# Optimization experiments

Measured on AMD Instinct MI355X. Metric: run time of the kernel, lower is better.

## Reference

```python
import jax, jax.numpy as jnp
import numpy as np
from functools import partial

S = 4096      # total tokens (single-request prefill)
H = 32        # indexer heads
D = 128       # indexer head dim (power of 2 for Hadamard)
R = 64        # rope head dim
QLR = 1536    # q_lora_rank
HID = 2048    # hidden size
TOPK = 2048   # index_topk
EPS = 1e-6
NEG = -1e30


def fwht(x):
    """Fast Walsh-Hadamard transform over last dim, scaled by d**-0.5."""
    d = x.shape[-1]
    orig = x.shape
    x = x.reshape(-1, d)
    h = 1
    while h < d:
        x = x.reshape(-1, d // (2 * h), 2, h)
        a, b = x[:, :, 0, :], x[:, :, 1, :]
        x = jnp.stack([a + b, a - b], axis=2).reshape(-1, d)
        h *= 2
    return (x * (d ** -0.5)).reshape(orig)


def apply_rope_interleaved(x, cos, sin):
    # non-neox (interleaved pairs): (x0,x1) -> (x0*c - x1*s, x0*s + x1*c)
    xe, xo = x[..., 0::2], x[..., 1::2]
    return jnp.stack([xe * cos - xo * sin, xe * sin + xo * cos], axis=-1).reshape(x.shape)


def setup_inputs() -> dict:
    key = jax.random.key(0)
    ks = jax.random.split(key, 8)
    hidden_states = jax.random.normal(ks[0], (S, HID), dtype=jnp.float32)
    q_lora = jax.random.normal(ks[1], (S, QLR), dtype=jnp.float32)
    positions = jnp.arange(S, dtype=jnp.int32)
    Wq = jax.random.normal(ks[2], (QLR, H * D), dtype=jnp.float32) * 0.02
    Wk = jax.random.normal(ks[3], (HID, D), dtype=jnp.float32) * 0.02
    k_gamma = jnp.ones((D,), dtype=jnp.float32)
    k_beta = jnp.zeros((D,), dtype=jnp.float32)
    Wp = jax.random.normal(ks[4], (HID, H), dtype=jnp.float32) * 0.02
    return {"hidden_states": hidden_states, "q_lora": q_lora, "positions": positions,
            "Wq": Wq, "Wk": Wk, "k_gamma": k_gamma, "k_beta": k_beta, "Wp": Wp}


def _indexer_logits(hidden_states, q_lora, Wq, Wk, k_gamma, k_beta, Wp, positions):
    # q projection: [S, QLR] @ [QLR, H*D] -> [S, H, D]
    q = (q_lora @ Wq).reshape(S, H, D)
    # k projection + layernorm: [S, D]
    k = hidden_states @ Wk
    mu = jnp.mean(k, axis=-1, keepdims=True)
    var = jnp.mean(jnp.square(k - mu), axis=-1, keepdims=True)
    k = (k - mu) * jax.lax.rsqrt(var + EPS) * k_gamma + k_beta
    # RoPE on first R dims (interleaved / non-neox style)
    half = R // 2
    inv_freq = 1.0 / (10000.0 ** (jnp.arange(half, dtype=jnp.float32) * 2.0 / R))
    ang = positions.astype(jnp.float32)[:, None] * inv_freq          # [S, half]
    cos, sin = jnp.cos(ang), jnp.sin(ang)
    q = q.at[..., :R].set(apply_rope_interleaved(q[..., :R], cos[:, None, :], sin[:, None, :]))
    k = k.at[..., :R].set(apply_rope_interleaved(k[..., :R], cos, sin))
    # Hadamard activation rotation
    q = fwht(q)
    k = fwht(k)
    # per-head gate: weights_proj(x) * n_heads^-0.5 * q_scale(=1) * softmax_scale
    w = (hidden_states @ Wp) * (H ** -0.5) * (D ** -0.5)             # [S, H]
    # logits[t, s] = sum_h w[t, h] * relu(q[t, h] . k[s]); scan over heads
    k_t = k.T                                                         # [D, S]
    def head_step(acc, inp):
        qh, wh = inp                                                  # [S, D], [S]
        return acc + wh[:, None] * jax.nn.relu(qh @ k_t), None
    logits, _ = jax.lax.scan(head_step, jnp.zeros((S, S), jnp.float32),
                             (q.transpose(1, 0, 2), w.T))
    # causal mask (ks=0, ke=t+1 per token for single-request prefill)
    idx = jnp.arange(S)
    logits = jnp.where(idx[None, :] <= idx[:, None], logits, NEG)
    return logits


def reference(hidden_states, q_lora, positions, Wq, Wk, k_gamma, k_beta, Wp):
    logits = _indexer_logits(hidden_states, q_lora, Wq, Wk, k_gamma, k_beta, Wp, positions)
    vals, topk_idx = jax.lax.top_k(logits, TOPK)                      # [S, TOPK]
    topk_idx = jnp.where(vals > NEG * 0.5, topk_idx, -1).astype(jnp.int32)
    return logits, topk_idx
```

## Files before the change

kernel.cpp:

```cpp
#include <hip/hip_runtime.h>
#include <hip/hip_bf16.h>
#include <math.h>

#define S 4096
#define H 32
#define D 128
#define QLR 1536
#define HID 2048
#define TOPK_N 2048
#define NEGF (-1e30f)
#define KW_N 160

typedef __attribute__((ext_vector_type(8))) short bf16x8;
typedef __attribute__((ext_vector_type(4))) float f32x4;

__device__ __forceinline__ void async_copy16(const void* g, void* l) {
    __builtin_amdgcn_global_load_lds(
        (const __attribute__((address_space(1))) unsigned int*)g,
        (__attribute__((address_space(3))) unsigned int*)l,
        16, 0, 0);
}

__device__ __forceinline__ unsigned short bf16bits(float f) {
    __hip_bfloat16 h = __float2bfloat16(f);
    return *(unsigned short*)&h;
}

__global__ __launch_bounds__(256) void cast_bf16_kernel(
    const float* __restrict__ in, __hip_bfloat16* __restrict__ out, int n4)
{
    int i = blockIdx.x * blockDim.x + threadIdx.x;
    if (i < n4) {
        float4 v = ((const float4*)in)[i];
        ushort4 pack;
        pack.x = bf16bits(v.x);
        pack.y = bf16bits(v.y);
        pack.z = bf16bits(v.z);
        pack.w = bf16bits(v.w);
        *(ushort4*)(out + (size_t)i * 4) = pack;
    }
}

__global__ __launch_bounds__(256) void zero_f32(float* __restrict__ p, int n)
{
    int i = blockIdx.x * blockDim.x + threadIdx.x;
    if (i < n) p[i] = 0.0f;
}

__global__ __launch_bounds__(256) void transpose_cast_kernel(
    const float* __restrict__ in, __hip_bfloat16* __restrict__ out)
{
    __shared__ float sm[32][33];
    const int nb = blockIdx.x;
    const int kb = blockIdx.y;
    const int t = threadIdx.x;
    const int j = t & 31, i0 = t >> 5;
#pragma unroll
    for (int u = 0; u < 4; ++u) {
        int i = i0 + u * 8;
        sm[i][j] = in[(size_t)(kb * 32 + i) * 4096 + nb * 32 + j];
    }
    __syncthreads();
#pragma unroll
    for (int u = 0; u < 4; ++u) {
        int i = i0 + u * 8;
        out[(size_t)(nb * 32 + i) * 1536 + kb * 32 + j] = __float2bfloat16(sm[j][i]);
    }
}

__global__ __launch_bounds__(256) void build_wkpT(
    const float* __restrict__ Wk, const float* __restrict__ Wp,
    __hip_bfloat16* __restrict__ WkpT)
{
    int g = blockIdx.x * blockDim.x + threadIdx.x;
    if (g >= KW_N * HID) return;
    int n = g / HID, k = g % HID;
    float v = (n < 128) ? Wk[(size_t)k * 128 + n]
                        : Wp[(size_t)k * 32 + (n - 128)] * 0.015625f;
    WkpT[g] = __float2bfloat16(v);
}

__global__ __launch_bounds__(256, 2) void kw_mfma(
    const short* __restrict__ hb,
    const short* __restrict__ WkpT,
    float* __restrict__ kf32,
    float* __restrict__ wbuf)
{
    const int mt = blockIdx.x;
    const int kc = blockIdx.y;
    const int tid = threadIdx.x;
    const int wave = tid >> 6, lane = tid & 63, grp = lane >> 4, lm = lane & 15;
    __shared__ short As[64 * 128];
    __shared__ short Bs[KW_N * 128];

    const int rhi = tid >> 4;
    const int e = (tid & 15) ^ rhi;

#pragma unroll
    for (int it = 0; it < 4; ++it) {
        int r = it * 16 + rhi;
        async_copy16(hb + (size_t)(mt * 64 + r) * HID + kc * 128 + e * 8,
                     (void*)(As + it * 2048 + wave * 512));
    }
#pragma unroll
    for (int it = 0; it < 10; ++it) {
        int r = it * 16 + rhi;
        async_copy16(WkpT + (size_t)r * HID + kc * 128 + e * 8,
                     (void*)(Bs + it * 2048 + wave * 512));
    }
    __syncthreads();

    f32x4 acc[10] = {};
#pragma unroll
    for (int k4 = 0; k4 < 4; ++k4) {
        int ch = ((k4 << 2) + grp) ^ lm;
        bf16x8 a = *(const bf16x8*)(As + (wave * 16 + lm) * 128 + ch * 8);
#pragma unroll
        for (int n = 0; n < 10; ++n) {
            bf16x8 b = *(const bf16x8*)(Bs + (n * 16 + lm) * 128 + ch * 8);
            acc[n] = __builtin_amdgcn_mfma_f32_16x16x32_bf16(a, b, acc[n], 0, 0, 0);
        }
    }

#pragma unroll
    for (int n = 0; n < 10; ++n) {
#pragma unroll
        for (int r = 0; r < 4; ++r) {
            int row = mt * 64 + wave * 16 + grp * 4 + r;
            int col = n * 16 + lm;
            if (n < 8) atomicAdd(&kf32[(size_t)row * 128 + col], acc[n][r]);
            else       atomicAdd(&wbuf[(size_t)row * 32 + (col - 128)], acc[n][r]);
        }
    }
}

__global__ __launch_bounds__(256, 2) void gemm_bf16_bt(
    const __hip_bfloat16* __restrict__ A, const __hip_bfloat16* __restrict__ BT,
    __hip_bfloat16* __restrict__ C, int M, int N, int K)
{
    __shared__ short As[128 * 32];
    __shared__ short Bs[128 * 32];
    const int tid = threadIdx.x;
    const int wave = tid >> 6, lane = tid & 63, grp = lane >> 4, lm = lane & 15;
    const int row0 = blockIdx.y * 128, col0 = blockIdx.x * 128;
    const short* Ag = (const short*)A;
    const short* Bg = (const short*)BT;

    f32x4 acc[2][8] = {};

    for (int kc = 0; kc < K; kc += 32) {
        __syncthreads();
#pragma unroll
        for (int is = 0; is < 2; ++is) {
            int r = is * 64 + (tid >> 2);
            async_copy16(Ag + (size_t)(row0 + r) * K + kc + (tid & 3) * 8,
                         (void*)(As + is * 2048 + wave * 512));
            async_copy16(Bg + (size_t)(col0 + r) * K + kc + (tid & 3) * 8,
                         (void*)(Bs + is * 2048 + wave * 512));
        }
        __syncthreads();
        bf16x8 a0 = *(const bf16x8*)(As + (wave * 32 + lm) * 32 + grp * 8);
        bf16x8 a1 = *(const bf16x8*)(As + (wave * 32 + 16 + lm) * 32 + grp * 8);
#pragma unroll
        for (int c = 0; c < 8; ++c) {
            bf16x8 b = *(const bf16x8*)(Bs + (c * 16 + lm) * 32 + grp * 8);
            acc[0][c] = __builtin_amdgcn_mfma_f32_16x16x32_bf16(a0, b, acc[0][c], 0, 0, 0);
            acc[1][c] = __builtin_amdgcn_mfma_f32_16x16x32_bf16(a1, b, acc[1][c], 0, 0, 0);
        }
    }
#pragma unroll
    for (int t = 0; t < 2; ++t)
#pragma unroll
        for (int c = 0; c < 8; ++c)
#pragma unroll
            for (int r = 0; r < 4; ++r) {
                int rr = row0 + wave * 32 + t * 16 + grp * 4 + r;
                int cc = col0 + c * 16 + lm;
                C[(size_t)rr * N + cc] = __float2bfloat16(acc[t][c][r]);
            }
}

__global__ void sincos_table_kernel(const int* __restrict__ positions,
                                    float* __restrict__ cosT, float* __restrict__ sinT)
{
    int g = blockIdx.x * blockDim.x + threadIdx.x;
    if (g >= S * 32) return;
    int s = g >> 5;
    int p = g & 31;
    double inv = pow(10000.0, -((double)(2 * p)) / 64.0);
    double ang = (double)positions[s] * inv;
    cosT[g] = (float)cos(ang);
    sinT[g] = (float)sin(ang);
}

__global__ __launch_bounds__(128) void post_kernel(
    const void* in, int in_bf16, __hip_bfloat16* outb,
    const float* __restrict__ cosT, const float* __restrict__ sinT,
    const float* __restrict__ gamma, const float* __restrict__ beta,
    int heads, int do_ln)
{
    const int row = blockIdx.x;
    const int t = threadIdx.x;
    const int srow = row / heads;
    __shared__ float sm[128];
    __shared__ float red[2];

    float v;
    if (in_bf16) v = __bfloat162float(((const __hip_bfloat16*)in)[(size_t)row * 128 + t]);
    else         v = ((const float*)in)[(size_t)row * 128 + t];

    if (do_ln) {
        float sv = v;
#pragma unroll
        for (int o = 32; o > 0; o >>= 1) sv += __shfl_down(sv, o);
        if ((t & 63) == 0) red[t >> 6] = sv;
        __syncthreads();
        float mu = (red[0] + red[1]) * (1.0f / 128.0f);
        __syncthreads();
        float d = v - mu;
        float sq = d * d;
#pragma unroll
        for (int o = 32; o > 0; o >>= 1) sq += __shfl_down(sq, o);
        if ((t & 63) == 0) red[t >> 6] = sq;
        __syncthreads();
        float var = (red[0] + red[1]) * (1.0f / 128.0f);
        v = d * rsqrtf(var + 1e-6f) * gamma[t] + beta[t];
        __syncthreads();
    }
    sm[t] = v;
    __syncthreads();

    if (t < 32) {
        float c = cosT[(size_t)srow * 32 + t];
        float sn = sinT[(size_t)srow * 32 + t];
        float xe = sm[2 * t];
        float xo = sm[2 * t + 1];
        sm[2 * t]     = xe * c - xo * sn;
        sm[2 * t + 1] = xe * sn + xo * c;
    }
    __syncthreads();

    for (int hstep = 1; hstep < 128; hstep <<= 1) {
        int i = 0; float a = 0.f, b = 0.f;
        bool act = (t < 64);
        if (act) {
            i = ((t & ~(hstep - 1)) << 1) | (t & (hstep - 1));
            a = sm[i];
            b = sm[i + hstep];
        }
        __syncthreads();
        if (act) { sm[i] = a + b; sm[i + hstep] = a - b; }
        __syncthreads();
    }
    outb[(size_t)row * 128 + t] = __float2bfloat16(sm[t] * 0.08838834764831845f);
}

__global__ __launch_bounds__(256, 2) void logits_mfma(
    const short* __restrict__ qb,
    const short* __restrict__ kb,
    const float* __restrict__ w,
    float* __restrict__ out)
{
    const int bx = blockIdx.x, by = blockIdx.y;
    const int row0 = by * 128, col0 = bx * 128;
    const int tid = threadIdx.x;

    if (bx > by) {
        const float4 n4 = make_float4(NEGF, NEGF, NEGF, NEGF);
        int c = (tid & 31) * 4;
        for (int r = tid >> 5; r < 128; r += 8)
            *(float4*)&out[(size_t)(row0 + r) * S + col0 + c] = n4;
        return;
    }

    __shared__ short As[128 * 128];
    __shared__ short Bs[128 * 128];
    const int wave = tid >> 6, lane = tid & 63, grp = lane >> 4, lm = lane & 15;
    const int rhi = tid >> 4;
    const int e = (tid & 15) ^ rhi;

#pragma unroll
    for (int it = 0; it < 8; ++it) {
        int r = it * 16 + rhi;
        async_copy16(kb + (size_t)(col0 + r) * D + e * 8,
                     (void*)(Bs + it * 2048 + wave * 512));
    }

    f32x4 accP[2][8] = {};

    for (int h = 0; h < H; ++h) {
        __syncthreads();
#pragma unroll
        for (int it = 0; it < 8; ++it) {
            int r = it * 16 + rhi;
            async_copy16(qb + (size_t)(row0 + r) * (H * D) + h * D + e * 8,
                         (void*)(As + it * 2048 + wave * 512));
        }
        float wv[2][4];
#pragma unroll
        for (int t = 0; t < 2; ++t)
#pragma unroll
            for (int r = 0; r < 4; ++r)
                wv[t][r] = w[(size_t)(row0 + wave * 32 + t * 16 + grp * 4 + r) * H + h];
        __syncthreads();

        f32x4 accH[2][8] = {};
#pragma unroll
        for (int kc = 0; kc < 4; ++kc) {
            int ch = ((kc << 2) + grp) ^ lm;
            bf16x8 a0 = *(const bf16x8*)(As + (wave * 32 + lm) * 128 + ch * 8);
            bf16x8 a1 = *(const bf16x8*)(As + (wave * 32 + 16 + lm) * 128 + ch * 8);
#pragma unroll
            for (int c = 0; c < 8; ++c) {
                bf16x8 b = *(const bf16x8*)(Bs + (c * 16 + lm) * 128 + ch * 8);
                accH[0][c] = __builtin_amdgcn_mfma_f32_16x16x32_bf16(a0, b, accH[0][c], 0, 0, 0);
                accH[1][c] = __builtin_amdgcn_mfma_f32_16x16x32_bf16(a1, b, accH[1][c], 0, 0, 0);
            }
        }
#pragma unroll
        for (int t = 0; t < 2; ++t)
#pragma unroll
            for (int c = 0; c < 8; ++c)
#pragma unroll
                for (int r = 0; r < 4; ++r)
                    accP[t][c][r] += wv[t][r] * fmaxf(accH[t][c][r], 0.0f);
    }

#pragma unroll
    for (int t = 0; t < 2; ++t)
#pragma unroll
        for (int c = 0; c < 8; ++c)
#pragma unroll
            for (int r = 0; r < 4; ++r) {
                int rr = row0 + wave * 32 + t * 16 + grp * 4 + r;
                int cc = col0 + c * 16 + lm;
                out[(size_t)rr * S + cc] = (cc <= rr) ? accP[t][c][r] : NEGF;
            }
}

__device__ __forceinline__ unsigned mono32(float f)
{
    unsigned u = __float_as_uint(f);
    return (u & 0x80000000u) ? ~u : (u | 0x80000000u);
}

__global__ __launch_bounds__(256) void topk_select(
    const float* __restrict__ logits, float* __restrict__ out_idx)
{
    const int row = blockIdx.x;
    const int tid = threadIdx.x;
    const int valid = row + 1;
    float* orow = out_idx + (size_t)row * TOPK_N;

    if (valid <= TOPK_N) {
        for (int p = tid; p < TOPK_N; p += 256)
            orow[p] = (p < valid) ? (float)p : -1.0f;
        return;
    }

    __shared__ float vals[S];
    __shared__ unsigned hist[2048];
    __shared__ unsigned chunk[256];
    __shared__ unsigned long long sh_prefix;
    __shared__ int sh_rem;
    __shared__ unsigned sh_cnt;

    const float* lr = logits + (size_t)row * S;
    for (int j = tid; j < valid; j += 256) vals[j] = lr[j];
    if (tid == 0) { sh_prefix = 0ull; sh_rem = TOPK_N; sh_cnt = 0u; }
    __syncthreads();

    for (int rnd = 0; rnd < 4; ++rnd) {
        const int shift = 33 - 11 * rnd;
        for (int i = tid; i < 2048; i += 256) hist[i] = 0u;
        __syncthreads();
        const unsigned long long pref = sh_prefix;
        const int rem = sh_rem;
        const int hs = shift + 11;
        for (int j = tid; j < valid; j += 256) {
            unsigned long long key = (((unsigned long long)mono32(vals[j])) << 12)
                                   | (unsigned)(4095 - j);
            if ((key >> hs) == (pref >> hs))
                atomicAdd(&hist[(unsigned)(key >> shift) & 2047u], 1u);
        }
        __syncthreads();
        unsigned csum = 0;
#pragma unroll
        for (int d = 0; d < 8; ++d) csum += hist[tid * 8 + d];
        chunk[tid] = csum;
        __syncthreads();
        for (int off = 1; off < 256; off <<= 1) {
            unsigned v = (tid + off < 256) ? chunk[tid + off] : 0u;
            __syncthreads();
            chunk[tid] += v;
            __syncthreads();
        }
        unsigned A = (tid < 255) ? chunk[tid + 1] : 0u;
        for (int dd = 7; dd >= 0; --dd) {
            unsigned c = hist[tid * 8 + dd];
            if (c && A < (unsigned)rem && (unsigned)rem <= A + c) {
                sh_prefix = pref | ((unsigned long long)(tid * 8 + dd) << shift);
                sh_rem = rem - (int)A;
            }
            A += c;
        }
        __syncthreads();
    }

    const unsigned long long Kstar = sh_prefix;
    for (int j = tid; j < valid; j += 256) {
        unsigned long long key = (((unsigned long long)mono32(vals[j])) << 12)
                               | (unsigned)(4095 - j);
        if (key >= Kstar) {
            unsigned p = atomicAdd(&sh_cnt, 1u);
            orow[p] = (float)j;
        }
    }
}

extern "C" void kernel_launch(void* const* d_in, const int* in_sizes, int n_in,
                              void* d_out, int out_size, void* d_ws, size_t ws_size,
                              hipStream_t stream)
{
    const float* hidden    = (const float*)d_in[0];
    const float* q_lora    = (const float*)d_in[1];
    const int*   positions = (const int*)d_in[2];
    const float* Wq        = (const float*)d_in[3];
    const float* Wk        = (const float*)d_in[4];
    const float* k_gamma   = (const float*)d_in[5];
    const float* k_beta    = (const float*)d_in[6];
    const float* Wp        = (const float*)d_in[7];

    char* ws = (char*)d_ws;
    size_t off = 0;
    __hip_bfloat16* qb16 = (__hip_bfloat16*)(ws + off); off += (size_t)S * H * D * 2;
    __hip_bfloat16* qlb  = (__hip_bfloat16*)(ws + off); off += (size_t)S * QLR * 2;
    __hip_bfloat16* WqT  = (__hip_bfloat16*)(ws + off); off += (size_t)(H * D) * QLR * 2;
    __hip_bfloat16* hb   = (__hip_bfloat16*)(ws + off); off += (size_t)S * HID * 2;
    __hip_bfloat16* WkpT = (__hip_bfloat16*)(ws + off); off += (size_t)KW_N * HID * 2;
    float* kf32 = (float*)(ws + off); off += (size_t)S * D * 4;
    __hip_bfloat16* kb16 = (__hip_bfloat16*)(ws + off); off += (size_t)S * D * 2;
    float* wbuf = (float*)(ws + off); off += (size_t)S * H * 4;
    float* cosT = (float*)(ws + off); off += (size_t)S * 32 * 4;
    float* sinT = (float*)(ws + off); off += (size_t)S * 32 * 4;

    float* out_logits = (float*)d_out;
    float* out_idx = out_logits + (size_t)S * S;

    cast_bf16_kernel<<<(S * QLR / 4 + 255) / 256, 256, 0, stream>>>(q_lora, qlb, S * QLR / 4);
    transpose_cast_kernel<<<dim3((H * D) / 32, QLR / 32), 256, 0, stream>>>(Wq, WqT);

    gemm_bf16_bt<<<dim3((H * D) / 128, S / 128), 256, 0, stream>>>(
        qlb, WqT, qb16, S, H * D, QLR);

    cast_bf16_kernel<<<(S * HID / 4 + 255) / 256, 256, 0, stream>>>(hidden, hb, S * HID / 4);
    build_wkpT<<<(KW_N * HID + 255) / 256, 256, 0, stream>>>(Wk, Wp, WkpT);
    zero_f32<<<(S * D + 255) / 256, 256, 0, stream>>>(kf32, S * D);
    zero_f32<<<(S * H + 255) / 256, 256, 0, stream>>>(wbuf, S * H);
    kw_mfma<<<dim3(S / 64, HID / 128), 256, 0, stream>>>(
        (const short*)hb, (const short*)WkpT, kf32, wbuf);

    sincos_table_kernel<<<(S * 32) / 256, 256, 0, stream>>>(positions, cosT, sinT);

    post_kernel<<<S, 128, 0, stream>>>(kf32, 0, kb16, cosT, sinT, k_gamma, k_beta, 1, 1);
    post_kernel<<<S * H, 128, 0, stream>>>(qb16, 1, qb16, cosT, sinT, nullptr, nullptr, H, 0);

    logits_mfma<<<dim3(S / 128, S / 128), 256, 0, stream>>>(
        (const short*)qb16, (const short*)kb16, wbuf, out_logits);

    topk_select<<<S, 256, 0, stream>>>(out_logits, out_idx);
}
```

Measured before the change: 507.1 us.

## Rewrite post-processing as wave-per-row shuffles; retile logits kernel with register-resident K

The LayerNorm/RoPE/Hadamard post kernel now runs one row per wavefront, each lane holding two elements. The reductions and butterfly stages use xor shuffles instead of shared memory and many block barriers. The logits kernel switches to 64x128 tiles with a 2x2 wave layout and loads the K fragments into registers once, so the inner head loop skips re-reading B from LDS. Occupancy hint rises to 3 blocks per CU. The cost is more register pressure and a finer causal-skip granularity, which adds blocks.

```diff
diff --git a/kernel.cpp b/kernel.cpp
--- a/kernel.cpp
+++ b/kernel.cpp
@@ -24,6 +24,11 @@
 __device__ __forceinline__ unsigned short bf16bits(float f) {
     __hip_bfloat16 h = __float2bfloat16(f);
     return *(unsigned short*)&h;
+}
+
+__device__ __forceinline__ float bits2f(unsigned short u) {
+    unsigned v = ((unsigned)u) << 16;
+    return __uint_as_float(v);
 }
 
 __global__ __launch_bounds__(256) void cast_bf16_kernel(
@@ -193,89 +198,91 @@
     sinT[g] = (float)sin(ang);
 }
 
-__global__ __launch_bounds__(128) void post_kernel(
-    const void* in, int in_bf16, __hip_bfloat16* outb,
+__global__ __launch_bounds__(256) void post_wave(
+    const void* __restrict__ in, int in_bf16, __hip_bfloat16* __restrict__ outb,
     const float* __restrict__ cosT, const float* __restrict__ sinT,
     const float* __restrict__ gamma, const float* __restrict__ beta,
-    int heads, int do_ln)
-{
-    const int row = blockIdx.x;
-    const int t = threadIdx.x;
+    int heads, int do_ln, int nrows)
+{
+    const int row = blockIdx.x * 4 + (threadIdx.x >> 6);
+    if (row >= nrows) return;
+    const int l = threadIdx.x & 63;
     const int srow = row / heads;
-    __shared__ float sm[128];
-    __shared__ float red[2];
-
-    float v;
-    if (in_bf16) v = __bfloat162float(((const __hip_bfloat16*)in)[(size_t)row * 128 + t]);
-    else         v = ((const float*)in)[(size_t)row * 128 + t];
+
+    float a, b;
+    if (in_bf16) {
+        unsigned pr = ((const unsigned*)in)[(size_t)row * 64 + l];
+        a = bits2f((unsigned short)(pr & 0xffff));
+        b = bits2f((unsigned short)(pr >> 16));
+    } else {
+        float2 v = ((const float2*)in)[(size_t)row * 64 + l];
+        a = v.x; b = v.y;
+    }
 
     if (do_ln) {
-        float sv = v;
-#pragma unroll
-        for (int o = 32; o > 0; o >>= 1) sv += __shfl_down(sv, o);
-        if ((t & 63) == 0) red[t >> 6] = sv;
-        __syncthreads();
-        float mu = (red[0] + red[1]) * (1.0f / 128.0f);
-        __syncthreads();
-        float d = v - mu;
-        float sq = d * d;
-#pragma unroll
-        for (int o = 32; o > 0; o >>= 1) sq += __shfl_down(sq, o);
-        if ((t & 63) == 0) red[t >> 6] = sq;
-        __syncthreads();
-        float var = (red[0] + red[1]) * (1.0f / 128.0f);
-        v = d * rsqrtf(var + 1e-6f) * gamma[t] + beta[t];
-        __syncthreads();
-    }
-    sm[t] = v;
-    __syncthreads();
-
-    if (t < 32) {
-        float c = cosT[(size_t)srow * 32 + t];
-        float sn = sinT[(size_t)srow * 32 + t];
-        float xe = sm[2 * t];
-        float xo = sm[2 * t + 1];
-        sm[2 * t]     = xe * c - xo * sn;
-        sm[2 * t + 1] = xe * sn + xo * c;
-    }
-    __syncthreads();
-
-    for (int hstep = 1; hstep < 128; hstep <<= 1) {
-        int i = 0; float a = 0.f, b = 0.f;
-        bool act = (t < 64);
-        if (act) {
-            i = ((t & ~(hstep - 1)) << 1) | (t & (hstep - 1));
-            a = sm[i];
-            b = sm[i + hstep];
-        }
-        __syncthreads();
-        if (act) { sm[i] = a + b; sm[i + hstep] = a - b; }
-        __syncthreads();
-    }
-    outb[(size_t)row * 128 + t] = __float2bfloat16(sm[t] * 0.08838834764831845f);
-}
-
-__global__ __launch_bounds__(256, 2) void logits_mfma(
+        float s = a + b;
+#pragma unroll
+        for (int o = 1; o < 64; o <<= 1) s += __shfl_xor(s, o);
+        float mu = s * (1.0f / 128.0f);
+        float da = a - mu, db = b - mu;
+        float sq = da * da + db * db;
+#pragma unroll
+        for (int o = 1; o < 64; o <<= 1) sq += __shfl_xor(sq, o);
+        float rs = rsqrtf(sq * (1.0f / 128.0f) + 1e-6f);
+        float2 g = ((const float2*)gamma)[l];
+        float2 bt = ((const float2*)beta)[l];
+        a = da * rs * g.x + bt.x;
+        b = db * rs * g.y + bt.y;
+    }
+
+    if (l < 32) {
+        float c = cosT[(size_t)srow * 32 + l];
+        float sn = sinT[(size_t)srow * 32 + l];
+        float xe = a, xo = b;
+        a = xe * c - xo * sn;
+        b = xe * sn + xo * c;
+    }
+
+    {
+        float na = a + b, nb = a - b;
+        a = na; b = nb;
+    }
+#pragma unroll
+    for (int m = 1; m < 64; m <<= 1) {
+        float pa = __shfl_xor(a, m);
+        float pb = __shfl_xor(b, m);
+        if (l & m) { a = pa - a; b = pb - b; }
+        else       { a = a + pa; b = b + pb; }
+    }
+
+    const float sc = 0.08838834764831845f;
+    unsigned outp = (unsigned)bf16bits(a * sc) | ((unsigned)bf16bits(b * sc) << 16);
+    ((unsigned*)outb)[(size_t)row * 64 + l] = outp;
+}
+
+__global__ __launch_bounds__(256, 3) void logits_mfma(
     const short* __restrict__ qb,
     const short* __restrict__ kb,
     const float* __restrict__ w,
     float* __restrict__ out)
 {
-    const int bx = blockIdx.x, by = blockIdx.y;
-    const int row0 = by * 128, col0 = bx * 128;
+    const int bx = blockIdx.x;
+    const int by = blockIdx.y;
+    const int row0 = by * 64, col0 = bx * 128;
     const int tid = threadIdx.x;
 
-    if (bx > by) {
+    if (2 * bx > by) {
         const float4 n4 = make_float4(NEGF, NEGF, NEGF, NEGF);
         int c = (tid & 31) * 4;
-        for (int r = tid >> 5; r < 128; r += 8)
+        for (int r = tid >> 5; r < 64; r += 8)
             *(float4*)&out[(size_t)(row0 + r) * S + col0 + c] = n4;
         return;
     }
 
-    __shared__ short As[128 * 128];
+    __shared__ short As[64 * 128];
     __shared__ short Bs[128 * 128];
     const int wave = tid >> 6, lane = tid & 63, grp = lane >> 4, lm = lane & 15;
+    const int wr = wave >> 1, wc = wave & 1;
     const int rhi = tid >> 4;
     const int e = (tid & 15) ^ rhi;
 
@@ -285,13 +292,22 @@
         async_copy16(kb + (size_t)(col0 + r) * D + e * 8,
                      (void*)(Bs + it * 2048 + wave * 512));
     }
-
-    f32x4 accP[2][8] = {};
+    __syncthreads();
+
+    bf16x8 bfrag[4][4];
+#pragma unroll
+    for (int c = 0; c < 4; ++c)
+#pragma unroll
+        for (int kc = 0; kc < 4; ++kc)
+            bfrag[c][kc] = *(const bf16x8*)(
+                Bs + (wc * 64 + c * 16 + lm) * 128 + (((kc << 2) + grp) ^ lm) * 8);
+
+    f32x4 accP[2][4] = {};
 
     for (int h = 0; h < H; ++h) {
         __syncthreads();
 #pragma unroll
-        for (int it = 0; it < 8; ++it) {
+        for (int it = 0; it < 4; ++it) {
             int r = it * 16 + rhi;
             async_copy16(qb + (size_t)(row0 + r) * (H * D) + h * D + e * 8,
                          (void*)(As + it * 2048 + wave * 512));
@@ -301,26 +317,25 @@
         for (int t = 0; t < 2; ++t)
 #pragma unroll
             for (int r = 0; r < 4; ++r)
-                wv[t][r] = w[(size_t)(row0 + wave * 32 + t * 16 + grp * 4 + r) * H + h];
-        __syncthreads();
-
-        f32x4 accH[2][8] = {};
+                wv[t][r] = w[(size_t)(row0 + wr * 32 + t * 16 + grp * 4 + r) * H + h];
+        __syncthreads();
+
+        f32x4 accH[2][4] = {};
 #pragma unroll
         for (int kc = 0; kc < 4; ++kc) {
             int ch = ((kc << 2) + grp) ^ lm;
-            bf16x8 a0 = *(const bf16x8*)(As + (wave * 32 + lm) * 128 + ch * 8);
-            bf16x8 a1 = *(const bf16x8*)(As + (wave * 32 + 16 + lm) * 128 + ch * 8);
-#pragma unroll
-            for (int c = 0; c < 8; ++c) {
-                bf16x8 b = *(const bf16x8*)(Bs + (c * 16 + lm) * 128 + ch * 8);
-                accH[0][c] = __builtin_amdgcn_mfma_f32_16x16x32_bf16(a0, b, accH[0][c], 0, 0, 0);
-                accH[1][c] = __builtin_amdgcn_mfma_f32_16x16x32_bf16(a1, b, accH[1][c], 0, 0, 0);
+            bf16x8 a0 = *(const bf16x8*)(As + (wr * 32 + lm) * 128 + ch * 8);
+            bf16x8 a1 = *(const bf16x8*)(As + (wr * 32 + 16 + lm) * 128 + ch * 8);
+#pragma unroll
+            for (int c = 0; c < 4; ++c) {
+                accH[0][c] = __builtin_amdgcn_mfma_f32_16x16x32_bf16(a0, bfrag[c][kc], accH[0][c], 0, 0, 0);
+                accH[1][c] = __builtin_amdgcn_mfma_f32_16x16x32_bf16(a1, bfrag[c][kc], accH[1][c], 0, 0, 0);
             }
         }
 #pragma unroll
         for (int t = 0; t < 2; ++t)
 #pragma unroll
-            for (int c = 0; c < 8; ++c)
+            for (int c = 0; c < 4; ++c)
 #pragma unroll
                 for (int r = 0; r < 4; ++r)
                     accP[t][c][r] += wv[t][r] * fmaxf(accH[t][c][r], 0.0f);
@@ -329,11 +344,11 @@
 #pragma unroll
     for (int t = 0; t < 2; ++t)
 #pragma unroll
-        for (int c = 0; c < 8; ++c)
+        for (int c = 0; c < 4; ++c)
 #pragma unroll
             for (int r = 0; r < 4; ++r) {
-                int rr = row0 + wave * 32 + t * 16 + grp * 4 + r;
-                int cc = col0 + c * 16 + lm;
+                int rr = row0 + wr * 32 + t * 16 + grp * 4 + r;
+                int cc = col0 + wc * 64 + c * 16 + lm;
                 out[(size_t)rr * S + cc] = (cc <= rr) ? accP[t][c][r] : NEGF;
             }
 }
@@ -462,10 +477,12 @@
 
     sincos_table_kernel<<<(S * 32) / 256, 256, 0, stream>>>(positions, cosT, sinT);
 
-    post_kernel<<<S, 128, 0, stream>>>(kf32, 0, kb16, cosT, sinT, k_gamma, k_beta, 1, 1);
-    post_kernel<<<S * H, 128, 0, stream>>>(qb16, 1, qb16, cosT, sinT, nullptr, nullptr, H, 0);
-
-    logits_mfma<<<dim3(S / 128, S / 128), 256, 0, stream>>>(
+    post_wave<<<(S + 3) / 4, 256, 0, stream>>>(
+        kf32, 0, kb16, cosT, sinT, k_gamma, k_beta, 1, 1, S);
+    post_wave<<<(S * H + 3) / 4, 256, 0, stream>>>(
+        qb16, 1, qb16, cosT, sinT, nullptr, nullptr, H, 0, S * H);
+
+    logits_mfma<<<dim3(S / 128, S / 64), 256, 0, stream>>>(
         (const short*)qb16, (const short*)kb16, wbuf, out_logits);
 
     topk_select<<<S, 256, 0, stream>>>(out_logits, out_idx);
```

After: 486.7 us. -4.0%, faster.
